# Kernel tuning notes

Measured on AMD Instinct MI355X. Metric: run time of the kernel, lower is better.

The kernel has to match this reference:

```python
import jax, jax.numpy as jnp
import numpy as np

N, E, H, R, A = 100000, 1600000, 128, 500, 16  # nodes, edges, hidden, reservoir, actions
LN_EPS = 1e-5

def setup_inputs() -> dict:
    key = jax.random.key(0)
    ks = jax.random.split(key, 8)
    return {
        "node_feats": jax.random.normal(ks[0], (N, 2), jnp.float32),
        "edge_index": jax.random.randint(ks[1], (2, E), 0, N, dtype=jnp.int32),
        "esn_state": jax.random.normal(ks[2], (1, R), jnp.float32),
        "gcn_w": jax.random.normal(ks[3], (2, H), jnp.float32) * 0.5,
        "gcn_b": jnp.zeros((H,), jnp.float32),
        "ln_w": jnp.ones((H,), jnp.float32),
        "ln_b": jnp.zeros((H,), jnp.float32),
        "fc1_w": jax.random.normal(ks[4], (H + R, H), jnp.float32) * 0.04,
        "fc1_b": jnp.zeros((H,), jnp.float32),
        "fc2_w": jax.random.normal(ks[5], (H, A), jnp.float32) * 0.08,
        "fc2_b": jnp.zeros((A,), jnp.float32),
    }

def reference(node_feats, edge_index, esn_state, gcn_w, gcn_b, ln_w, ln_b,
              fc1_w, fc1_b, fc2_w, fc2_b):
    src, dst = edge_index[0], edge_index[1]
    n = node_feats.shape[0]
    # GCNConv: linear transform, then symmetric-normalized aggregation with self-loops
    h = node_feats @ gcn_w  # [N, H]
    deg = jax.ops.segment_sum(jnp.ones_like(src, dtype=h.dtype), dst, num_segments=n) + 1.0
    dis = jax.lax.rsqrt(deg)  # deg >= 1 due to self-loops
    norm = dis[src] * dis[dst]  # [E]
    agg = jax.ops.segment_sum(h[src] * norm[:, None], dst, num_segments=n)  # [N, H]
    x = agg + h * (dis * dis)[:, None] + gcn_b  # self-loop term + bias
    x = jax.nn.relu(x)
    # PyG LayerNorm, mode='graph', batch=None: normalize over all nodes & channels
    x = x - x.mean()
    x = x / (jnp.sqrt(x.var()) + LN_EPS)
    x = x * ln_w + ln_b
    pooled = x.sum(axis=0, keepdims=True)  # global_add_pool, single graph -> [1, H]
    z = jnp.concatenate([pooled, esn_state], axis=1)  # [1, H+R]
    z = jax.nn.relu(z @ fc1_w + fc1_b)
    logits = z @ fc2_w + fc2_b  # [1, A]
    return jax.nn.log_softmax(logits, axis=1)
```

## Files before the change

### kernel.cpp

```cpp
#include <hip/hip_runtime.h>
#include <math.h>

#define NN 100000
#define EE 1600000
#define HH 128
#define RR 500
#define AA 16
#define LN_EPS 1e-5f

#define BSH 8
#define NPB 256
#define NB 391
#define MAXPB 4608
#define EPW 8192
#define SCT 512
#define NWG_SC ((EE + EPW - 1) / EPW)
#define NZW 64

__global__ __launch_bounds__(256) void k_init_esn(unsigned int* __restrict__ zero_region,
                                                  const float* __restrict__ esn,
                                                  const float* __restrict__ fc1_w,
                                                  float* __restrict__ zpart) {
    const int w = blockIdx.x, t = threadIdx.x;
    if (w == 0) {
        for (int j = t; j < 642; j += 256) zero_region[j] = 0u;
        return;
    }
    const int sl = w - 1;
    const int k0 = sl * 8;
    const int k1 = min(k0 + 8, RR);
    if (t < HH) {
        float acc = 0.f;
        for (int k = k0; k < k1; ++k)
            acc = fmaf(esn[k], fc1_w[(size_t)(HH + k) * HH + t], acc);
        zpart[(size_t)sl * HH + t] = acc;
    }
}

__global__ __launch_bounds__(SCT) void k_scatter(const int* __restrict__ src,
                                                 const int* __restrict__ dst,
                                                 unsigned int* __restrict__ gctr,
                                                 unsigned int* __restrict__ payload) {
    __shared__ unsigned int hist[512], rank[512], hbase[512];
    const int t = threadIdx.x;
    hist[t] = 0u; rank[t] = 0u; hbase[t] = 0u;
    __syncthreads();
    const int e0 = blockIdx.x * EPW;
    const int ecnt = max(0, min(EPW, EE - e0));
    const int nv = ecnt >> 2;
    const int4* d4 = reinterpret_cast<const int4*>(dst + e0);
    const int4* s4 = reinterpret_cast<const int4*>(src + e0);

    for (int k = t; k < nv; k += SCT) {
        int4 d = d4[k];
        atomicAdd(&hist[((unsigned)d.x) >> BSH], 1u);
        atomicAdd(&hist[((unsigned)d.y) >> BSH], 1u);
        atomicAdd(&hist[((unsigned)d.z) >> BSH], 1u);
        atomicAdd(&hist[((unsigned)d.w) >> BSH], 1u);
    }
    __syncthreads();

    if (t < NB && hist[t] > 0u) hbase[t] = atomicAdd(&gctr[t], hist[t]);
    __syncthreads();

    for (int k = t; k < nv; k += SCT) {
        int4 d = d4[k];
        int4 s = s4[k];
        #define EMIT(SS, DD) { \
            unsigned int dd = (unsigned)(DD), ss = (unsigned)(SS); \
            unsigned int b = dd >> BSH; \
            unsigned int r = atomicAdd(&rank[b], 1u); \
            unsigned int slot = hbase[b] + r; \
            if (slot < MAXPB) payload[(size_t)b * MAXPB + slot] = (ss << BSH) | (dd & (NPB - 1)); }
        EMIT(s.x, d.x) EMIT(s.y, d.y) EMIT(s.z, d.z) EMIT(s.w, d.w)
        #undef EMIT
    }
}

__global__ __launch_bounds__(1024) void k_bdeg_g(const unsigned int* __restrict__ gctr,
                                                 const unsigned int* __restrict__ payload,
                                                 const float* __restrict__ nf,
                                                 float* __restrict__ rsv, float* __restrict__ g) {
    __shared__ unsigned int hist[NPB];
    const int b = blockIdx.x, t = threadIdx.x;
    if (t < NPB) hist[t] = 0u;
    __syncthreads();
    const unsigned int cnt = min(gctr[b], (unsigned int)MAXPB);
    const unsigned int* pl = payload + (size_t)b * MAXPB;
    const uint4* pl4 = reinterpret_cast<const uint4*>(pl);
    const unsigned int nv = cnt >> 2;
    for (unsigned int k = t; k < nv; k += 1024) {
        uint4 p = pl4[k];
        atomicAdd(&hist[p.x & (NPB - 1)], 1u);
        atomicAdd(&hist[p.y & (NPB - 1)], 1u);
        atomicAdd(&hist[p.z & (NPB - 1)], 1u);
        atomicAdd(&hist[p.w & (NPB - 1)], 1u);
    }
    for (unsigned int k = (nv << 2) + t; k < cnt; k += 1024)
        atomicAdd(&hist[pl[k] & (NPB - 1)], 1u);
    __syncthreads();
    if (t < NPB) {
        int node = (b << BSH) + t;
        if (node < NN) {
            float df = 1.0f + (float)hist[t];
            float rs = rsqrtf(df);
            rsv[node] = rs;
            float2 f = *reinterpret_cast<const float2*>(&nf[2 * node]);
            float2 gv; gv.x = rs * f.x; gv.y = rs * f.y;
            *reinterpret_cast<float2*>(&g[2 * node]) = gv;
        }
    }
}

__global__ __launch_bounds__(1024) void k_bagg_node(const unsigned int* __restrict__ gctr,
        const unsigned int* __restrict__ payload,
        const float* __restrict__ g, const float* __restrict__ rsv,
        const float* __restrict__ gcn_w, const float* __restrict__ gcn_b,
        float* __restrict__ S, float* __restrict__ T2, unsigned int* __restrict__ done,
        const float* __restrict__ zpart,
        const float* __restrict__ ln_w, const float* __restrict__ ln_b,
        const float* __restrict__ fc1_w, const float* __restrict__ fc1_b,
        const float* __restrict__ fc2_w, const float* __restrict__ fc2_b,
        float* __restrict__ out) {
    __shared__ union {
        struct { float agg[NPB * 2]; float shSf[HH]; float shw[16]; } ba;
        struct { float psum[8][HH]; float pooled[HH]; float z[HH];
                 float logits[AA]; float red[2]; } fin;
    } u;
    __shared__ int s_last;
    const int b = blockIdx.x, t = threadIdx.x;
    if (t < NPB * 2) u.ba.agg[t] = 0.f;
    if (t < HH) u.ba.shSf[t] = 0.f;
    __syncthreads();
    const unsigned int cnt = min(gctr[b], (unsigned int)MAXPB);
    const unsigned int* pl = payload + (size_t)b * MAXPB;
    const uint4* pl4 = reinterpret_cast<const uint4*>(pl);
    const unsigned int nv = cnt >> 2;
    for (unsigned int k = t; k < nv; k += 1024) {
        uint4 p = pl4[k];
        #define ACC(P) { \
            unsigned int s = (P) >> BSH, dl = (P) & (NPB - 1); \
            float2 gv = *reinterpret_cast<const float2*>(&g[2 * s]); \
            atomicAdd(&u.ba.agg[dl],       gv.x); \
            atomicAdd(&u.ba.agg[NPB + dl], gv.y); }
        ACC(p.x) ACC(p.y) ACC(p.z) ACC(p.w)
        #undef ACC
    }
    for (unsigned int k = (nv << 2) + t; k < cnt; k += 1024) {
        unsigned int p = pl[k];
        unsigned int s = p >> BSH, dl = p & (NPB - 1);
        float2 gv = *reinterpret_cast<const float2*>(&g[2 * s]);
        atomicAdd(&u.ba.agg[dl],       gv.x);
        atomicAdd(&u.ba.agg[NPB + dl], gv.y);
    }
    __syncthreads();

    const int nvalid = min(NPB, NN - (b << BSH));
    if (t < nvalid) {
        int node = (b << BSH) + t;
        float rs = rsv[node];
        float2 gv = *reinterpret_cast<const float2*>(&g[2 * node]);
        u.ba.agg[t]       = rs * (u.ba.agg[t]       + gv.x);
        u.ba.agg[NPB + t] = rs * (u.ba.agg[NPB + t] + gv.y);
    }
    __syncthreads();

    const int ch = t & (HH - 1), slot = t >> 7;
    {
        const float w0 = gcn_w[ch], w1 = gcn_w[HH + ch], bb = gcn_b[ch];
        float accS = 0.f, accT2 = 0.f;
        for (int j = slot; j < nvalid; j += 8) {
            float x = fmaf(u.ba.agg[j], w0, fmaf(u.ba.agg[NPB + j], w1, bb));
            float r = fmaxf(x, 0.f);
            accS  += r;
            accT2 += r * r;
        }
        atomicAdd(&u.ba.shSf[ch], accS);
        float v = accT2;
        for (int o = 32; o; o >>= 1) v += __shfl_down(v, o, 64);
        if ((t & 63) == 0) u.ba.shw[t >> 6] = v;
        __syncthreads();
        if (t < HH) atomicAdd(&S[t], u.ba.shSf[t]);
        if (t == 0) {
            float s2 = 0.f;
            #pragma unroll
            for (int w = 0; w < 16; ++w) s2 += u.ba.shw[w];
            atomicAdd(T2, s2);
        }
    }
    __syncthreads();
    if (t == 0) {
        unsigned int old = atomicAdd(done, 1u);
        s_last = (old == NB - 1) ? 1 : 0;
    }
    __syncthreads();
    if (!s_last) return;

    const int sl = t >> 7;
    if (t < HH) {
        float s = __hip_atomic_load(&S[t], __ATOMIC_RELAXED, __HIP_MEMORY_SCOPE_AGENT);
        u.fin.pooled[t] = s;
        float vv = s;
        for (int o = 32; o; o >>= 1) vv += __shfl_down(vv, o, 64);
        if ((t & 63) == 0) u.fin.red[t >> 6] = vv;
    }
    __syncthreads();
    const float T1 = u.fin.red[0] + u.fin.red[1];
    const float T2v = __hip_atomic_load(T2, __ATOMIC_RELAXED, __HIP_MEMORY_SCOPE_AGENT);
    const float cntf = (float)NN * (float)HH;
    const float mean = T1 / cntf;
    const float var  = T2v / cntf - mean * mean;
    const float denom = sqrtf(var) + LN_EPS;
    if (t < HH)
        u.fin.pooled[t] = ln_w[t] * (u.fin.pooled[t] - (float)NN * mean) / denom + (float)NN * ln_b[t];
    __syncthreads();

    float acc = 0.f;
    for (int k = sl * 16; k < sl * 16 + 16; ++k)
        acc = fmaf(u.fin.pooled[k], fc1_w[(size_t)k * HH + ch], acc);
    for (int w = sl * 8; w < sl * 8 + 8; ++w)
        acc += zpart[(size_t)w * HH + ch];
    u.fin.psum[sl][ch] = acc;
    __syncthreads();
    if (t < HH) {
        float a = fc1_b[t];
        #pragma unroll
        for (int k = 0; k < 8; ++k) a += u.fin.psum[k][t];
        u.fin.z[t] = fmaxf(a, 0.f);
    }
    __syncthreads();

    if (t < AA) {
        float l = fc2_b[t];
        for (int j = 0; j < HH; ++j)
            l = fmaf(u.fin.z[j], fc2_w[j * AA + t], l);
        u.fin.logits[t] = l;
    }
    __syncthreads();

    if (t == 0) {
        float m = u.fin.logits[0];
        for (int a = 1; a < AA; ++a) m = fmaxf(m, u.fin.logits[a]);
        float sum = 0.f;
        for (int a = 0; a < AA; ++a) sum += expf(u.fin.logits[a] - m);
        float lse = m + logf(sum);
        for (int a = 0; a < AA; ++a) out[a] = u.fin.logits[a] - lse;
    }
}


__global__ void k_initf(unsigned int* __restrict__ p, int n) {
    int i = blockIdx.x * blockDim.x + threadIdx.x;
    int stride = gridDim.x * blockDim.x;
    for (int j = i; j < n; j += stride) p[j] = 0u;
}

__global__ void k_deg1(const int* __restrict__ dst, int* __restrict__ deg, int e) {
    int i = blockIdx.x * blockDim.x + threadIdx.x;
    if (i < e) atomicAdd(&deg[dst[i]], 1);
}

__global__ void k_g1(const int* __restrict__ deg, const float* __restrict__ nf,
                     float* __restrict__ degf, float* __restrict__ g, int n) {
    int i = blockIdx.x * blockDim.x + threadIdx.x;
    if (i < n) {
        float df = (float)(1 + deg[i]);
        degf[i] = df;
        float rs = rsqrtf(df);
        float2 f = *reinterpret_cast<const float2*>(&nf[2 * i]);
        float2 gv; gv.x = rs * f.x; gv.y = rs * f.y;
        *reinterpret_cast<float2*>(&g[2 * i]) = gv;
    }
}

__global__ void k_edge1(const int* __restrict__ src, const int* __restrict__ dst,
                        const float* __restrict__ g, float* __restrict__ B, int e) {
    int i = blockIdx.x * blockDim.x + threadIdx.x;
    if (i < e) {
        int s = src[i], d = dst[i];
        float2 gv = *reinterpret_cast<const float2*>(&g[2 * s]);
        atomicAdd(&B[2 * d],     gv.x);
        atomicAdd(&B[2 * d + 1], gv.y);
    }
}

__global__ void k_node(const float* __restrict__ nf, const float* __restrict__ degf,
                       const float* __restrict__ B,
                       const float* __restrict__ gcn_w, const float* __restrict__ gcn_b,
                       float* __restrict__ S, float* __restrict__ T2, int n) {
    const int ch   = threadIdx.x & (HH - 1);
    const int slot = threadIdx.x >> 7;
    const float w0 = gcn_w[ch];
    const float w1 = gcn_w[HH + ch];
    const float b  = gcn_b[ch];
    float accS = 0.f, accT2 = 0.f;
    for (int i = blockIdx.x * 2 + slot; i < n; i += gridDim.x * 2) {
        float df   = degf[i];
        float invd = 1.0f / df;
        float rs   = rsqrtf(df);
        float2 bv = *reinterpret_cast<const float2*>(&B[2 * i]);
        float2 f  = *reinterpret_cast<const float2*>(&nf[2 * i]);
        float b0 = rs * bv.x + f.x * invd;
        float b1 = rs * bv.y + f.y * invd;
        float xv = fmaf(b0, w0, fmaf(b1, w1, b));
        float r  = fmaxf(xv, 0.f);
        accS  += r;
        accT2 += r * r;
    }
    __shared__ float shS[HH];
    if (slot == 1) shS[ch] = accS;
    __syncthreads();
    if (slot == 0) atomicAdd(&S[ch], accS + shS[ch]);
    float v = accT2;
    for (int o = 32; o; o >>= 1) v += __shfl_down(v, o, 64);
    __shared__ float shw[4];
    if ((threadIdx.x & 63) == 0) shw[threadIdx.x >> 6] = v;
    __syncthreads();
    if (threadIdx.x == 0) atomicAdd(T2, shw[0] + shw[1] + shw[2] + shw[3]);
}

__global__ void k_final(const float* __restrict__ S, const float* __restrict__ T2ptr,
                        const float* __restrict__ esn,
                        const float* __restrict__ ln_w, const float* __restrict__ ln_b,
                        const float* __restrict__ fc1_w, const float* __restrict__ fc1_b,
                        const float* __restrict__ fc2_w, const float* __restrict__ fc2_b,
                        float* __restrict__ out) {
    const int t = threadIdx.x;
    __shared__ float sh_pooled[HH];
    __shared__ float sh_z[HH];
    __shared__ float sh_logits[AA];
    __shared__ float shred[2];

    float s = S[t];
    float v = s;
    for (int o = 32; o; o >>= 1) v += __shfl_down(v, o, 64);
    if ((t & 63) == 0) shred[t >> 6] = v;
    __syncthreads();
    const float T1 = shred[0] + shred[1];
    const float T2 = *T2ptr;
    const float cnt = (float)NN * (float)HH;
    const float mean = T1 / cnt;
    const float var  = T2 / cnt - mean * mean;
    const float denom = sqrtf(var) + LN_EPS;
    sh_pooled[t] = ln_w[t] * (s - (float)NN * mean) / denom + (float)NN * ln_b[t];
    __syncthreads();

    float acc = fc1_b[t];
    for (int k = 0; k < HH; ++k)
        acc = fmaf(sh_pooled[k], fc1_w[k * HH + t], acc);
    for (int k = 0; k < RR; ++k)
        acc = fmaf(esn[k], fc1_w[(HH + k) * HH + t], acc);
    sh_z[t] = fmaxf(acc, 0.f);
    __syncthreads();

    if (t < AA) {
        float l = fc2_b[t];
        for (int j = 0; j < HH; ++j)
            l = fmaf(sh_z[j], fc2_w[j * AA + t], l);
        sh_logits[t] = l;
    }
    __syncthreads();

    if (t == 0) {
        float m = sh_logits[0];
        for (int a = 1; a < AA; ++a) m = fmaxf(m, sh_logits[a]);
        float sum = 0.f;
        for (int a = 0; a < AA; ++a) sum += expf(sh_logits[a] - m);
        float lse = m + logf(sum);
        for (int a = 0; a < AA; ++a) out[a] = sh_logits[a] - lse;
    }
}

extern "C" void kernel_launch(void* const* d_in, const int* in_sizes, int n_in,
                              void* d_out, int out_size, void* d_ws, size_t ws_size,
                              hipStream_t stream) {
    const float* nf     = (const float*)d_in[0];
    const int*   ei     = (const int*)d_in[1];
    const float* esn    = (const float*)d_in[2];
    const float* gcn_w  = (const float*)d_in[3];
    const float* gcn_b  = (const float*)d_in[4];
    const float* ln_w   = (const float*)d_in[5];
    const float* ln_b   = (const float*)d_in[6];
    const float* fc1_w  = (const float*)d_in[7];
    const float* fc1_b  = (const float*)d_in[8];
    const float* fc2_w  = (const float*)d_in[9];
    const float* fc2_b  = (const float*)d_in[10];
    float* out = (float*)d_out;
    float* ws  = (float*)d_ws;

    const size_t OFF_S       = 512;
    const size_t OFF_T2      = OFF_S + HH;
    const size_t OFF_DONE    = OFF_T2 + 1;
    const size_t OFF_ZPART   = 644;
    const size_t OFF_PAYLOAD = OFF_ZPART + (size_t)NZW * HH;
    const size_t OFF_RSV     = OFF_PAYLOAD + (size_t)NB * MAXPB;
    const size_t OFF_G       = OFF_RSV + NN;
    const size_t NEED_BKT    = (OFF_G + 2 * (size_t)NN) * 4;

    if (ws_size >= NEED_BKT) {
        unsigned int* gctr    = (unsigned int*)ws;
        float*        S       = ws + OFF_S;
        float*        T2      = ws + OFF_T2;
        unsigned int* done    = (unsigned int*)ws + OFF_DONE;
        float*        zpart   = ws + OFF_ZPART;
        unsigned int* payload = (unsigned int*)ws + OFF_PAYLOAD;
        float*        rsv     = ws + OFF_RSV;
        float*        g       = ws + OFF_G;

        hipLaunchKernelGGL(k_init_esn,  dim3(NZW + 1), dim3(256),  0, stream, (unsigned int*)ws, esn, fc1_w, zpart);
        hipLaunchKernelGGL(k_scatter,   dim3(NWG_SC),  dim3(SCT),  0, stream, ei, ei + EE, gctr, payload);
        hipLaunchKernelGGL(k_bdeg_g,    dim3(NB),      dim3(1024), 0, stream, gctr, payload, nf, rsv, g);
        hipLaunchKernelGGL(k_bagg_node, dim3(NB),      dim3(1024), 0, stream,
                           gctr, payload, g, rsv, gcn_w, gcn_b, S, T2, done, zpart,
                           ln_w, ln_b, fc1_w, fc1_b, fc2_w, fc2_b, out);
    } else {
        int*   deg  = (int*)ws;
        float* B    = ws + NN;
        float* S    = ws + 3 * (size_t)NN;
        float* T2   = ws + 3 * (size_t)NN + 128;
        float* degf = ws + 3 * (size_t)NN + 130;
        float* g    = ws + 4 * (size_t)NN + 130;
        const int eb = (EE + 255) / 256;
        const int nb = (NN + 255) / 256;
        hipLaunchKernelGGL(k_initf, dim3(2048), dim3(256), 0, stream, (unsigned int*)ws, 3 * NN + 129);
        hipLaunchKernelGGL(k_deg1,  dim3(eb),   dim3(256), 0, stream, ei + EE, deg, EE);
        hipLaunchKernelGGL(k_g1,    dim3(nb),   dim3(256), 0, stream, deg, nf, degf, g, NN);
        hipLaunchKernelGGL(k_edge1, dim3(eb),   dim3(256), 0, stream, ei, ei + EE, g, B, EE);
        hipLaunchKernelGGL(k_node,  dim3(512),  dim3(256), 0, stream, nf, degf, B, gcn_w, gcn_b, S, T2, NN);
        hipLaunchKernelGGL(k_final, dim3(1),    dim3(128), 0, stream,
                           S, T2, esn, ln_w, ln_b, fc1_w, fc1_b, fc2_w, fc2_b, out);
    }
}
```

Measured before the change: 66.12 us.

## Fuse histogram and rank passes in edge scatter, holding edges in registers

The scatter kernel now uses 1024 threads, and each thread holds its two int4 edge chunks in registers. A single pass of LDS atomics on the rank array serves as both the per-bucket histogram and the local rank, which removes the separate histogram pass and the second global read of dst and src. After the global base reservation, each thread writes its payloads from registers. This costs more registers per thread, and the register-held design assumes EPW equals 8 times SCT.

Result: no change. 66.12 us (+0.0%).

```diff
diff --git a/kernel.cpp b/kernel.cpp
--- a/kernel.cpp
+++ b/kernel.cpp
@@ -13,7 +13,7 @@
 #define NB 391
 #define MAXPB 4608
 #define EPW 8192
-#define SCT 512
+#define SCT 1024
 #define NWG_SC ((EE + EPW - 1) / EPW)
 #define NZW 64
 
@@ -41,9 +41,9 @@
                                                  const int* __restrict__ dst,
                                                  unsigned int* __restrict__ gctr,
                                                  unsigned int* __restrict__ payload) {
-    __shared__ unsigned int hist[512], rank[512], hbase[512];
+    __shared__ unsigned int rank[512], hbase[512];
     const int t = threadIdx.x;
-    hist[t] = 0u; rank[t] = 0u; hbase[t] = 0u;
+    if (t < 512) { rank[t] = 0u; hbase[t] = 0u; }
     __syncthreads();
     const int e0 = blockIdx.x * EPW;
     const int ecnt = max(0, min(EPW, EE - e0));
@@ -51,29 +51,41 @@
     const int4* d4 = reinterpret_cast<const int4*>(dst + e0);
     const int4* s4 = reinterpret_cast<const int4*>(src + e0);
 
-    for (int k = t; k < nv; k += SCT) {
-        int4 d = d4[k];
-        atomicAdd(&hist[((unsigned)d.x) >> BSH], 1u);
-        atomicAdd(&hist[((unsigned)d.y) >> BSH], 1u);
-        atomicAdd(&hist[((unsigned)d.z) >> BSH], 1u);
-        atomicAdd(&hist[((unsigned)d.w) >> BSH], 1u);
-    }
-    __syncthreads();
-
-    if (t < NB && hist[t] > 0u) hbase[t] = atomicAdd(&gctr[t], hist[t]);
-    __syncthreads();
-
-    for (int k = t; k < nv; k += SCT) {
-        int4 d = d4[k];
-        int4 s = s4[k];
-        #define EMIT(SS, DD) { \
-            unsigned int dd = (unsigned)(DD), ss = (unsigned)(SS); \
-            unsigned int b = dd >> BSH; \
-            unsigned int r = atomicAdd(&rank[b], 1u); \
-            unsigned int slot = hbase[b] + r; \
-            if (slot < MAXPB) payload[(size_t)b * MAXPB + slot] = (ss << BSH) | (dd & (NPB - 1)); }
-        EMIT(s.x, d.x) EMIT(s.y, d.y) EMIT(s.z, d.z) EMIT(s.w, d.w)
-        #undef EMIT
+    unsigned int pw[8], pbr[8];
+    bool vk[2];
+
+    #pragma unroll
+    for (int kk = 0; kk < 2; ++kk) {
+        const int k = t + kk * SCT;
+        vk[kk] = (k < nv);
+        if (vk[kk]) {
+            int4 d = d4[k];
+            int4 s = s4[k];
+            #define GRAB(i, SS, DD) { \
+                unsigned int dd = (unsigned)(DD), ss = (unsigned)(SS); \
+                unsigned int b = dd >> BSH; \
+                unsigned int r = atomicAdd(&rank[b], 1u); \
+                pw[kk * 4 + i]  = (ss << BSH) | (dd & (NPB - 1)); \
+                pbr[kk * 4 + i] = (b << 16) | (r & 0xFFFFu); }
+            GRAB(0, s.x, d.x) GRAB(1, s.y, d.y) GRAB(2, s.z, d.z) GRAB(3, s.w, d.w)
+            #undef GRAB
+        }
+    }
+    __syncthreads();
+
+    if (t < NB && rank[t] > 0u) hbase[t] = atomicAdd(&gctr[t], rank[t]);
+    __syncthreads();
+
+    #pragma unroll
+    for (int kk = 0; kk < 2; ++kk) {
+        if (vk[kk]) {
+            #define PUT(i) { \
+                unsigned int b = pbr[kk * 4 + i] >> 16; \
+                unsigned int slot = hbase[b] + (pbr[kk * 4 + i] & 0xFFFFu); \
+                if (slot < MAXPB) payload[(size_t)b * MAXPB + slot] = pw[kk * 4 + i]; }
+            PUT(0) PUT(1) PUT(2) PUT(3)
+            #undef PUT
+        }
     }
 }
 
```
